# Kernel optimization log

Measured on AMD Instinct MI355X. Metric: run time of the kernel, lower is better.

Reference implementation:

```python
import jax, jax.numpy as jnp
import numpy as np

B, S, E, H = 2, 2048, 1024, 16
D = E // H  # head_dim = 64


def _rope_angles(seq_len, d, dtype=jnp.float32):
    # standard RoPE frequencies: theta_i = 10000^{-2i/d}
    inv_freq = 1.0 / (10000.0 ** (jnp.arange(0, d, 2, dtype=dtype) / d))  # [d/2]
    pos = jnp.arange(seq_len, dtype=dtype)                                # [S]
    ang = pos[:, None] * inv_freq[None, :]                                # [S, d/2]
    ang = jnp.concatenate([ang, ang], axis=-1)                            # [S, d]
    return jnp.cos(ang), jnp.sin(ang)


def _rotate_half(t):
    t1, t2 = jnp.split(t, 2, axis=-1)
    return jnp.concatenate([-t2, t1], axis=-1)


def _apply_rope(t, cos, sin):
    # t: [B, H, S, D]; cos/sin: [S, D]
    return t * cos[None, None, :, :] + _rotate_half(t) * sin[None, None, :, :]


def setup_inputs() -> dict:
    key = jax.random.key(0)
    ks = jax.random.split(key, 6)
    x = jax.random.normal(ks[0], (B, S, E), dtype=jnp.float32)
    mask = jnp.tril(jnp.ones((S, S), dtype=bool))  # causal: True = attend
    scale = 1.0 / np.sqrt(E)
    Wq = jax.random.normal(ks[1], (E, E), dtype=jnp.float32) * scale
    Wk = jax.random.normal(ks[2], (E, E), dtype=jnp.float32) * scale
    Wv = jax.random.normal(ks[3], (E, E), dtype=jnp.float32) * scale
    Wo = jax.random.normal(ks[4], (E, E), dtype=jnp.float32) * scale
    z = jnp.zeros((E,), dtype=jnp.float32)
    return {"x": x, "mask": mask, "Wq": Wq, "bq": z, "Wk": Wk, "bk": z,
            "Wv": Wv, "bv": z, "Wo": Wo, "bo": z}


def reference(x, mask, Wq, bq, Wk, bk, Wv, bv, Wo, bo):
    b, s, e = x.shape
    # QKV projections (nn.Linear convention: y = x @ W.T + b)
    def proj(W, bias):
        y = jnp.einsum('bse,fe->bsf', x, W) + bias
        return y.reshape(b, s, H, D).transpose(0, 2, 1, 3)  # [B,H,S,D]
    q, k, v = proj(Wq, bq), proj(Wk, bk), proj(Wv, bv)
    # RoPE on q and k (per-head rotary over head_dim)
    cos, sin = _rope_angles(s, D, dtype=x.dtype)
    q = _apply_rope(q, cos, sin)
    k = _apply_rope(k, cos, sin)
    # SDPA with boolean mask (True = attend)
    scores = jnp.einsum('bhqd,bhkd->bhqk', q, k) / jnp.sqrt(jnp.asarray(D, x.dtype))
    neg = jnp.asarray(jnp.finfo(x.dtype).min, x.dtype)
    scores = jnp.where(mask[None, None, :, :], scores, neg)
    attn = jax.nn.softmax(scores, axis=-1)
    out = jnp.einsum('bhqk,bhkd->bhqd', attn, v)          # [B,H,S,D]
    out = out.transpose(0, 2, 1, 3).reshape(b, s, e)       # [B,S,E]
    return jnp.einsum('bse,fe->bsf', out, Wo) + bo
```

## Files before the change

### kernel.cpp

```cpp
#include <hip/hip_runtime.h>
#include <hip/hip_bf16.h>

typedef unsigned short u16;
typedef unsigned int u32;
typedef __bf16 bf16x8 __attribute__((ext_vector_type(8)));
typedef float f32x4 __attribute__((ext_vector_type(4)));

#define S_LEN 2048
#define NHEAD 16
#define HDIM  64
#define EMB   1024
#define BATCH 2

__device__ __forceinline__ float bf2f(u16 u) {
  union { unsigned int i; float f; } c; c.i = ((unsigned int)u) << 16; return c.f;
}
__device__ __forceinline__ u16 f2bf(float f) {
  union { float f; unsigned int i; } c; c.f = f;
  unsigned int i = c.i;
  return (u16)((i + 0x7FFFu + ((i >> 16) & 1u)) >> 16);
}
__device__ __forceinline__ u16 f2bf_trunc(float f) {
  union { float f; unsigned int i; } c; c.f = f;
  return (u16)(c.i >> 16);
}
__device__ __forceinline__ f32x4 mfma16(bf16x8 a, bf16x8 b, f32x4 c) {
  return __builtin_amdgcn_mfma_f32_16x16x32_bf16(a, b, c, 0, 0, 0);
}
__device__ __forceinline__ void cp16(const u16* g, u16* l) {
  __builtin_amdgcn_global_load_lds(
      (const __attribute__((address_space(1))) u32*)g,
      (__attribute__((address_space(3))) u32*)l, 16, 0, 0);
}

__global__ __launch_bounds__(256) void convert_kernel(
    const void* __restrict__ x, const void* __restrict__ Wq,
    const void* __restrict__ Wk, const void* __restrict__ Wv,
    const void* __restrict__ Wo,
    u16* __restrict__ xb, u16* __restrict__ wqb, u16* __restrict__ wkb,
    u16* __restrict__ wvb, u16* __restrict__ wob,
    int* __restrict__ flag, float2* __restrict__ tab)
{
  __shared__ int s_flag;
  if (threadIdx.x == 0) s_flag = 0;
  __syncthreads();
  {
    const u16* xs = (const u16*)x;
    u16 w0 = xs[threadIdx.x * 2], w1 = xs[threadIdx.x * 2 + 1];
    if ((((w0 >> 7) & 0xFF) >= 0xC0) || (((w1 >> 7) & 0xFF) >= 0xC0))
      atomicOr(&s_flag, 1);
  }
  __syncthreads();
  const int f32io = s_flag;
  if (blockIdx.x == 0 && threadIdx.x == 0) flag[0] = f32io;

  size_t gid = (size_t)blockIdx.x * 256 + threadIdx.x;
  size_t e = gid * 8;
  const void* src; u16* dst; size_t off;
  if (e < 4194304) { src = x; dst = xb; off = e; }
  else {
    size_t rr = e - 4194304;
    int j = (int)(rr >> 20); off = rr & 1048575;
    src = (j == 0) ? Wq : (j == 1) ? Wk : (j == 2) ? Wv : Wo;
    dst = (j == 0) ? wqb : (j == 1) ? wkb : (j == 2) ? wvb : wob;
  }
  if (f32io) {
    const float* s = (const float*)src + off;
    float4 a = *(const float4*)s;
    float4 b2 = *(const float4*)(s + 4);
    ushort4 u0; u0.x = f2bf(a.x); u0.y = f2bf(a.y); u0.z = f2bf(a.z); u0.w = f2bf(a.w);
    ushort4 u1; u1.x = f2bf(b2.x); u1.y = f2bf(b2.y); u1.z = f2bf(b2.z); u1.w = f2bf(b2.w);
    *(ushort4*)(dst + off) = u0;
    *(ushort4*)(dst + off + 4) = u1;
  } else {
    *(uint4*)(dst + off) = *(const uint4*)((const u16*)src + off);
  }

  if (blockIdx.x < 256) {
    int id = blockIdx.x * 256 + threadIdx.x;
    int s = id >> 5, i = id & 31;
    float f = exp2f(-(float)i * 0.41524101186092029f);
    float ang = (float)s * f;
    tab[id] = make_float2(cosf(ang), sinf(ang));
  }
}

__device__ __forceinline__ void gemm_core_db(
    const u16* __restrict__ A, const u16* __restrict__ W,
    int m0, int n0, int t, f32x4 (&acc)[4][4],
    u16* __restrict__ Ash, u16* __restrict__ Bsh)
{
  const int lane = t & 63, lr = lane & 15, quad = lane >> 4;
  const int wv = t >> 6;
  const int wm = (wv & 1) * 64, wn = (wv >> 1) * 64;
  const int r0 = t >> 2, c0 = (t & 3) * 8;
  const int r1 = (t + 256) >> 2, c1 = (t & 3) * 8;
  const int lds0 = (t & 192) * 8;
  const int lds1 = (256 + (t & 192)) * 8;
  const u16* gA0 = A + (size_t)(m0 + r0) * 1024 + c0;
  const u16* gA1 = A + (size_t)(m0 + r1) * 1024 + c1;
  const u16* gB0 = W + (size_t)(n0 + r0) * 1024 + c0;
  const u16* gB1 = W + (size_t)(n0 + r1) * 1024 + c1;

  cp16(gA0, Ash + lds0); cp16(gA1, Ash + lds1);
  cp16(gB0, Bsh + lds0); cp16(gB1, Bsh + lds1);
  __syncthreads();

  for (int kt = 0; kt < 1024; kt += 32) {
    const int cur = (kt >> 5) & 1;
    const u16* Ac = Ash + cur * 4096;
    const u16* Bc = Bsh + cur * 4096;
    bf16x8 af[4], bfr[4];
#pragma unroll
    for (int mi = 0; mi < 4; ++mi)
      af[mi] = *(const bf16x8*)(Ac + (wm + mi * 16 + lr) * 32 + quad * 8);
#pragma unroll
    for (int ni = 0; ni < 4; ++ni)
      bfr[ni] = *(const bf16x8*)(Bc + (wn + ni * 16 + lr) * 32 + quad * 8);
    if (kt + 32 < 1024) {
      u16* An = Ash + (1 - cur) * 4096;
      u16* Bn = Bsh + (1 - cur) * 4096;
      cp16(gA0 + kt + 32, An + lds0); cp16(gA1 + kt + 32, An + lds1);
      cp16(gB0 + kt + 32, Bn + lds0); cp16(gB1 + kt + 32, Bn + lds1);
    }
#pragma unroll
    for (int mi = 0; mi < 4; ++mi)
#pragma unroll
      for (int ni = 0; ni < 4; ++ni)
        acc[mi][ni] = mfma16(af[mi], bfr[ni], acc[mi][ni]);
    __syncthreads();
  }
}

__device__ __forceinline__ void gemm_epilogue(
    int mode, int f32io, f32x4 (&acc)[4][4],
    const void* biasvp, void* outvp, int m0, int n0, int t,
    const float2* __restrict__ tab)
{
  const int lane = t & 63, lr = lane & 15, quad = lane >> 4;
  const int wv = t >> 6;
  const int wm = (wv & 1) * 64, wn = (wv >> 1) * 64;
  const float* biasf = (const float*)biasvp;
  const u16* biasb = (const u16*)biasvp;
#define BIASV(n) (f32io ? biasf[(n)] : bf2f(biasb[(n)]))
  if (mode == 1) {
    u16* Out = (u16*)outvp;
#pragma unroll
    for (int mi = 0; mi < 4; ++mi) {
#pragma unroll
      for (int r = 0; r < 4; ++r) {
        int mm = m0 + wm + mi * 16 + quad * 4 + r;
        int s = mm & (S_LEN - 1), b = mm >> 11;
        float2 cs0 = tab[s * 32 + lr];
        float2 cs1 = tab[s * 32 + 16 + lr];
#pragma unroll
        for (int ni = 0; ni < 4; ++ni) {
          int n = n0 + wn + ni * 16 + lr;
          int h = n >> 6, d = n & 63;
          float v  = acc[mi][ni][r]     + BIASV(n);
          float vp = acc[mi][ni ^ 2][r] + BIASV(n ^ 32);
          float rot = (d < 32) ? -vp : vp;
          float cc = (ni & 1) ? cs1.x : cs0.x;
          float ss = (ni & 1) ? cs1.y : cs0.y;
          size_t off = (((size_t)(b * NHEAD + h)) * S_LEN + s) * HDIM + d;
          Out[off] = f2bf(v * cc + rot * ss);
        }
      }
    }
  } else if (mode == 2) {
    u16* Out = (u16*)outvp;
#pragma unroll
    for (int mi = 0; mi < 4; ++mi) {
      int mm = m0 + wm + mi * 16 + quad * 4;
      int s = mm & (S_LEN - 1), b = mm >> 11;
#pragma unroll
      for (int ni = 0; ni < 4; ++ni) {
        int n = n0 + wn + ni * 16 + lr;
        int h = n >> 6, d = n & 63;
        float bv = BIASV(n);
        u16 p0 = f2bf(acc[mi][ni][0] + bv);
        u16 p1 = f2bf(acc[mi][ni][1] + bv);
        u16 p2 = f2bf(acc[mi][ni][2] + bv);
        u16 p3 = f2bf(acc[mi][ni][3] + bv);
        uint2 pk = make_uint2((u32)p0 | ((u32)p1 << 16),
                              (u32)p2 | ((u32)p3 << 16));
        size_t off = (((size_t)(b * NHEAD + h)) * HDIM + d) * S_LEN + s;
        *(uint2*)(Out + off) = pk;
      }
    }
  }
#undef BIASV
}

__global__ __launch_bounds__(256) void gemm_qkv(
    const u16* __restrict__ A, const u16* __restrict__ Wq,
    const u16* __restrict__ Wk, const u16* __restrict__ Wv,
    const void* bq, const void* bk, const void* bv,
    u16* qo, u16* ko, u16* vo, const int* __restrict__ dflag,
    const float2* __restrict__ tab)
{
  alignas(16) __shared__ u16 Ash[2 * 128 * 32];
  alignas(16) __shared__ u16 Bsh[2 * 128 * 32];
  const int wsel = blockIdx.x >> 3;
  const u16* W = (wsel == 0) ? Wq : (wsel == 1) ? Wk : Wv;
  const void* bias = (wsel == 0) ? bq : (wsel == 1) ? bk : bv;
  void* out = (wsel == 0) ? (void*)qo : (wsel == 1) ? (void*)ko : (void*)vo;
  const int mode = (wsel == 2) ? 2 : 1;
  const int m0 = blockIdx.y * 128, n0 = (blockIdx.x & 7) * 128;
  f32x4 acc[4][4];
  const f32x4 zero4 = {0.f, 0.f, 0.f, 0.f};
#pragma unroll
  for (int i = 0; i < 4; ++i)
#pragma unroll
    for (int j = 0; j < 4; ++j) acc[i][j] = zero4;
  gemm_core_db(A, W, m0, n0, threadIdx.x, acc, Ash, Bsh);
  gemm_epilogue(mode, dflag[0], acc, bias, out, m0, n0, threadIdx.x, tab);
}

__global__ __launch_bounds__(256) void gemm_out(
    const u16* __restrict__ A, const u16* __restrict__ W,
    const void* bias, void* out, const int* __restrict__ dflag)
{
  alignas(16) __shared__ u16 Ash[2 * 64 * 32];
  alignas(16) __shared__ u16 Bsh[2 * 128 * 32];
  const int t = threadIdx.x, lane = t & 63, wv = t >> 6;
  const int lr = lane & 15, quad = lane >> 4;
  const int m0 = blockIdx.y * 64, n0 = blockIdx.x * 128;
  const int wm = (wv & 1) * 32, wn = (wv >> 1) * 64;
  const int f32io = dflag[0];

  const int r0 = t >> 2, c0 = (t & 3) * 8;
  const int r1 = (t + 256) >> 2;
  const int lds0 = (t & 192) * 8;
  const int lds1 = (256 + (t & 192)) * 8;
  const u16* gA0 = A + (size_t)(m0 + (r0 & 63)) * 1024 + c0;
  const u16* gB0 = W + (size_t)(n0 + r0) * 1024 + c0;
  const u16* gB1 = W + (size_t)(n0 + r1) * 1024 + c0;

  f32x4 acc[2][4];
  const f32x4 zero4 = {0.f, 0.f, 0.f, 0.f};
#pragma unroll
  for (int i = 0; i < 2; ++i)
#pragma unroll
    for (int j = 0; j < 4; ++j) acc[i][j] = zero4;

  cp16(gA0, Ash + lds0);
  cp16(gB0, Bsh + lds0); cp16(gB1, Bsh + lds1);
  __syncthreads();

  for (int kt = 0; kt < 1024; kt += 32) {
    const int cur = (kt >> 5) & 1;
    const u16* Ac = Ash + cur * 2048;
    const u16* Bc = Bsh + cur * 4096;
    bf16x8 af[2], bfr[4];
#pragma unroll
    for (int mi = 0; mi < 2; ++mi)
      af[mi] = *(const bf16x8*)(Ac + (wm + mi * 16 + lr) * 32 + quad * 8);
#pragma unroll
    for (int ni = 0; ni < 4; ++ni)
      bfr[ni] = *(const bf16x8*)(Bc + (wn + ni * 16 + lr) * 32 + quad * 8);
    if (kt + 32 < 1024) {
      u16* An = Ash + (1 - cur) * 2048;
      u16* Bn = Bsh + (1 - cur) * 4096;
      cp16(gA0 + kt + 32, An + lds0);
      cp16(gB0 + kt + 32, Bn + lds0); cp16(gB1 + kt + 32, Bn + lds1);
    }
#pragma unroll
    for (int mi = 0; mi < 2; ++mi)
#pragma unroll
      for (int ni = 0; ni < 4; ++ni)
        acc[mi][ni] = mfma16(af[mi], bfr[ni], acc[mi][ni]);
    __syncthreads();
  }

  const float* biasf = (const float*)bias;
  const u16* biasb = (const u16*)bias;
  float* Outf = (float*)out;
  u16* Outb = (u16*)out;
#pragma unroll
  for (int mi = 0; mi < 2; ++mi) {
#pragma unroll
    for (int r = 0; r < 4; ++r) {
      int mm = m0 + wm + mi * 16 + quad * 4 + r;
#pragma unroll
      for (int ni = 0; ni < 4; ++ni) {
        int n = n0 + wn + ni * 16 + lr;
        float bv = f32io ? biasf[n] : bf2f(biasb[n]);
        float v = acc[mi][ni][r] + bv;
        size_t off = (size_t)mm * 1024 + n;
        if (f32io) Outf[off] = v; else Outb[off] = f2bf(v);
      }
    }
  }
}

__device__ __forceinline__ void attn_phase(
    const bf16x8 (&qf)[2], f32x4 (&oacc)[4], float& lsum,
    u16 (&Ksh)[64][72], u16 (&Vsh)[64][72], u16 (&Psh)[4][16][72],
    int kv0, int q0w, bool diag, int lr, int quad, int wv)
{
  const f32x4 zero4 = {0.f, 0.f, 0.f, 0.f};
  f32x4 sc[4];
#pragma unroll
  for (int ni = 0; ni < 4; ++ni) {
    bf16x8 kf0 = *(const bf16x8*)&Ksh[ni * 16 + lr][quad * 8];
    bf16x8 kf1 = *(const bf16x8*)&Ksh[ni * 16 + lr][32 + quad * 8];
    f32x4 z = zero4;
    z = mfma16(kf0, qf[0], z);
    z = mfma16(kf1, qf[1], z);
    sc[ni] = z;
  }
  const int qa = q0w + lr;
  if (diag) {
#pragma unroll
    for (int ni = 0; ni < 4; ++ni)
#pragma unroll
      for (int r = 0; r < 4; ++r) {
        float sarg = sc[ni][r] * 0.18033688f - 21.64042561f;
        if (kv0 + ni * 16 + quad * 4 + r > qa) sarg = -1e4f;
        float p = exp2f(sarg);
        sc[ni][r] = p;
        lsum += p;
      }
  } else {
#pragma unroll
    for (int ni = 0; ni < 4; ++ni)
#pragma unroll
      for (int r = 0; r < 4; ++r) {
        float p = exp2f(sc[ni][r] * 0.18033688f - 21.64042561f);
        sc[ni][r] = p;
        lsum += p;
      }
  }
#pragma unroll
  for (int ni = 0; ni < 4; ++ni) {
    u32 lo = (u32)f2bf_trunc(sc[ni][0]) | ((u32)f2bf_trunc(sc[ni][1]) << 16);
    u32 hi = (u32)f2bf_trunc(sc[ni][2]) | ((u32)f2bf_trunc(sc[ni][3]) << 16);
    *(uint2*)&Psh[wv][lr][ni * 16 + quad * 4] = make_uint2(lo, hi);
  }
  bf16x8 pa0 = *(const bf16x8*)&Psh[wv][lr][quad * 8];
  bf16x8 pa1 = *(const bf16x8*)&Psh[wv][lr][32 + quad * 8];
#pragma unroll
  for (int oni = 0; oni < 4; ++oni) {
    bf16x8 vf0 = *(const bf16x8*)&Vsh[oni * 16 + lr][quad * 8];
    bf16x8 vf1 = *(const bf16x8*)&Vsh[oni * 16 + lr][32 + quad * 8];
    oacc[oni] = mfma16(pa0, vf0, oacc[oni]);
    oacc[oni] = mfma16(pa1, vf1, oacc[oni]);
  }
}

__device__ __forceinline__ void attn_finish(
    f32x4 (&oacc)[4], float lsum, u16* __restrict__ O,
    int bh, int q0w, int lr, int quad)
{
  const int b = bh >> 4, h = bh & 15;
  lsum += __shfl_xor(lsum, 16);
  lsum += __shfl_xor(lsum, 32);
  const float inv = 1.f / lsum;
#pragma unroll
  for (int r = 0; r < 4; ++r) {
    const float scale = __shfl(inv, quad * 4 + r);
#pragma unroll
    for (int oni = 0; oni < 4; ++oni) {
      int s = q0w + quad * 4 + r;
      int e = h * HDIM + oni * 16 + lr;
      O[((size_t)(b * S_LEN + s)) * EMB + e] = f2bf(oacc[oni][r] * scale);
    }
  }
}

__global__ __launch_bounds__(256) void attn_kernel(
    const u16* __restrict__ Q, const u16* __restrict__ Kr,
    const u16* __restrict__ Vt, u16* __restrict__ O)
{
  alignas(16) __shared__ u16 Ksh[64][72];
  alignas(16) __shared__ u16 Vsh[64][72];
  alignas(16) __shared__ u16 Psh[4][16][72];
  const int t = threadIdx.x, lane = t & 63, wv = t >> 6;
  const int lr = lane & 15, quad = lane >> 4;
  const int bh = blockIdx.y;
  const int xs = blockIdx.x;
  const int myTile = (xs >> 4) ? (xs & 15) : 31 - (xs & 15);
  const int q0w = myTile * 64 + wv * 16;
  const size_t base = (size_t)bh * S_LEN * HDIM;

  bf16x8 qf[2];
  {
    const u16* qrow = Q + base + (size_t)(q0w + lr) * HDIM + quad * 8;
    qf[0] = *(const bf16x8*)qrow;
    qf[1] = *(const bf16x8*)(qrow + 32);
  }

  f32x4 oacc[4];
  float lsum = 0.f;
  const f32x4 zero4 = {0.f, 0.f, 0.f, 0.f};
#pragma unroll
  for (int i = 0; i < 4; ++i) oacc[i] = zero4;

  const int rr = t >> 3, cc = (t & 7) * 8;
  uint4 krg0 = *(const uint4*)(Kr + base + (size_t)rr * HDIM + cc);
  uint4 krg1 = *(const uint4*)(Kr + base + (size_t)(rr + 32) * HDIM + cc);
  uint4 vrg0 = *(const uint4*)(Vt + base + (size_t)rr * S_LEN + cc);
  uint4 vrg1 = *(const uint4*)(Vt + base + (size_t)(rr + 32) * S_LEN + cc);

  for (int j = 0; j <= myTile; ++j) {
    __syncthreads();
    *(uint4*)&Ksh[rr][cc] = krg0;
    *(uint4*)&Ksh[rr + 32][cc] = krg1;
    *(uint4*)&Vsh[rr][cc] = vrg0;
    *(uint4*)&Vsh[rr + 32][cc] = vrg1;
    __syncthreads();
    if (j < myTile) {
      const int kv1 = (j + 1) * 64;
      krg0 = *(const uint4*)(Kr + base + (size_t)(kv1 + rr) * HDIM + cc);
      krg1 = *(const uint4*)(Kr + base + (size_t)(kv1 + rr + 32) * HDIM + cc);
      vrg0 = *(const uint4*)(Vt + base + (size_t)rr * S_LEN + kv1 + cc);
      vrg1 = *(const uint4*)(Vt + base + (size_t)(rr + 32) * S_LEN + kv1 + cc);
    }
    attn_phase(qf, oacc, lsum, Ksh, Vsh, Psh, j * 64, q0w, j == myTile,
               lr, quad, wv);
  }

  attn_finish(oacc, lsum, O, bh, q0w, lr, quad);
}

extern "C" void kernel_launch(void* const* d_in, const int* in_sizes, int n_in,
                              void* d_out, int out_size, void* d_ws, size_t ws_size,
                              hipStream_t stream) {
  const void* x  = d_in[0];
  const void* Wq = d_in[2]; const void* bq = d_in[3];
  const void* Wk = d_in[4]; const void* bk = d_in[5];
  const void* Wv = d_in[6]; const void* bv = d_in[7];
  const void* Wo = d_in[8]; const void* bo = d_in[9];

  char* ws = (char*)d_ws;
  int* flag = (int*)ws;
  u16* xb  = (u16*)(ws + 256);
  u16* qws = xb  + 4194304;
  u16* kws = qws + 4194304;
  u16* vws = kws + 4194304;
  u16* wqb = vws + 4194304;
  u16* wkb = wqb + 1048576;
  u16* wvb = wkb + 1048576;
  u16* wob = wvb + 1048576;
  float2* tab = (float2*)(wob + 1048576);
  u16* ows = xb;

  convert_kernel<<<4096, 256, 0, stream>>>(x, Wq, Wk, Wv, Wo,
                                           xb, wqb, wkb, wvb, wob, flag, tab);
  gemm_qkv<<<dim3(24, 32), 256, 0, stream>>>(xb, wqb, wkb, wvb,
                                             bq, bk, bv, qws, kws, vws, flag, tab);
  attn_kernel<<<dim3(32, 32), 256, 0, stream>>>(qws, kws, vws, ows);
  gemm_out<<<dim3(8, 64), 256, 0, stream>>>(ows, wob, bo, d_out, flag);
}
```

Baseline: 241.4 us.

## Pair causal query tiles per 512-thread block with split-KV work balancing

Each attention block now handles two query tiles (qtA and 31-qtA) with 8 waves. Once group A's short tile finishes, its waves split the remaining long-tile KV blocks with group B by halves of the key dimension, and the partial outputs are merged through shared memory. K/V shared tiles are double-buffered so there is one barrier per iteration instead of two. This targets causal load imbalance and the cost of synchronisation, at the price of higher register and LDS use per block and an extra reduction step at the end.

Result: faster. 208.5 us (-13.6%).

```diff
diff --git a/kernel.cpp b/kernel.cpp
--- a/kernel.cpp
+++ b/kernel.cpp
@@ -296,8 +296,9 @@
 
 __device__ __forceinline__ void attn_phase(
     const bf16x8 (&qf)[2], f32x4 (&oacc)[4], float& lsum,
-    u16 (&Ksh)[64][72], u16 (&Vsh)[64][72], u16 (&Psh)[4][16][72],
-    int kv0, int q0w, bool diag, int lr, int quad, int wv)
+    const u16 (*__restrict__ Ksh)[72], const u16 (*__restrict__ Vsh)[72],
+    u16 (*__restrict__ Pw)[72],
+    int kv0, int q0w, bool diag, int lr, int quad)
 {
   const f32x4 zero4 = {0.f, 0.f, 0.f, 0.f};
   f32x4 sc[4];
@@ -336,10 +337,10 @@
   for (int ni = 0; ni < 4; ++ni) {
     u32 lo = (u32)f2bf_trunc(sc[ni][0]) | ((u32)f2bf_trunc(sc[ni][1]) << 16);
     u32 hi = (u32)f2bf_trunc(sc[ni][2]) | ((u32)f2bf_trunc(sc[ni][3]) << 16);
-    *(uint2*)&Psh[wv][lr][ni * 16 + quad * 4] = make_uint2(lo, hi);
-  }
-  bf16x8 pa0 = *(const bf16x8*)&Psh[wv][lr][quad * 8];
-  bf16x8 pa1 = *(const bf16x8*)&Psh[wv][lr][32 + quad * 8];
+    *(uint2*)&Pw[lr][ni * 16 + quad * 4] = make_uint2(lo, hi);
+  }
+  bf16x8 pa0 = *(const bf16x8*)&Pw[lr][quad * 8];
+  bf16x8 pa1 = *(const bf16x8*)&Pw[lr][32 + quad * 8];
 #pragma unroll
   for (int oni = 0; oni < 4; ++oni) {
     bf16x8 vf0 = *(const bf16x8*)&Vsh[oni * 16 + lr][quad * 8];
@@ -349,6 +350,60 @@
   }
 }
 
+__device__ __forceinline__ void attn_phase_half(
+    const bf16x8 (&qf)[2], f32x4 (&oacc)[4], float& lsum,
+    const u16 (*__restrict__ Ksh)[72], const u16 (*__restrict__ Vsh)[72],
+    u16 (*__restrict__ Pw)[72],
+    int kv0, int q0w, bool diag, int half, int lr, int quad)
+{
+  const f32x4 zero4 = {0.f, 0.f, 0.f, 0.f};
+  f32x4 sc[2];
+#pragma unroll
+  for (int i = 0; i < 2; ++i) {
+    const int ni = half * 2 + i;
+    bf16x8 kf0 = *(const bf16x8*)&Ksh[ni * 16 + lr][quad * 8];
+    bf16x8 kf1 = *(const bf16x8*)&Ksh[ni * 16 + lr][32 + quad * 8];
+    f32x4 z = zero4;
+    z = mfma16(kf0, qf[0], z);
+    z = mfma16(kf1, qf[1], z);
+    sc[i] = z;
+  }
+  const int qa = q0w + lr;
+  if (diag) {
+#pragma unroll
+    for (int i = 0; i < 2; ++i)
+#pragma unroll
+      for (int r = 0; r < 4; ++r) {
+        float sarg = sc[i][r] * 0.18033688f - 21.64042561f;
+        if (kv0 + (half * 2 + i) * 16 + quad * 4 + r > qa) sarg = -1e4f;
+        float p = exp2f(sarg);
+        sc[i][r] = p;
+        lsum += p;
+      }
+  } else {
+#pragma unroll
+    for (int i = 0; i < 2; ++i)
+#pragma unroll
+      for (int r = 0; r < 4; ++r) {
+        float p = exp2f(sc[i][r] * 0.18033688f - 21.64042561f);
+        sc[i][r] = p;
+        lsum += p;
+      }
+  }
+#pragma unroll
+  for (int i = 0; i < 2; ++i) {
+    u32 lo = (u32)f2bf_trunc(sc[i][0]) | ((u32)f2bf_trunc(sc[i][1]) << 16);
+    u32 hi = (u32)f2bf_trunc(sc[i][2]) | ((u32)f2bf_trunc(sc[i][3]) << 16);
+    *(uint2*)&Pw[lr][(half * 2 + i) * 16 + quad * 4] = make_uint2(lo, hi);
+  }
+  bf16x8 pa = *(const bf16x8*)&Pw[lr][half * 32 + quad * 8];
+#pragma unroll
+  for (int oni = 0; oni < 4; ++oni) {
+    bf16x8 vf = *(const bf16x8*)&Vsh[oni * 16 + lr][half * 32 + quad * 8];
+    oacc[oni] = mfma16(pa, vf, oacc[oni]);
+  }
+}
+
 __device__ __forceinline__ void attn_finish(
     f32x4 (&oacc)[4], float lsum, u16* __restrict__ O,
     int bh, int q0w, int lr, int quad)
@@ -369,59 +424,87 @@
   }
 }
 
-__global__ __launch_bounds__(256) void attn_kernel(
+__global__ __launch_bounds__(512, 4) void attn_kernel(
     const u16* __restrict__ Q, const u16* __restrict__ Kr,
     const u16* __restrict__ Vt, u16* __restrict__ O)
 {
-  alignas(16) __shared__ u16 Ksh[64][72];
-  alignas(16) __shared__ u16 Vsh[64][72];
-  alignas(16) __shared__ u16 Psh[4][16][72];
+  alignas(16) __shared__ u16 Kdb[2][64][72];
+  alignas(16) __shared__ u16 Vdb[2][64][72];
+  alignas(16) __shared__ u16 Psh[8][16][72];
   const int t = threadIdx.x, lane = t & 63, wv = t >> 6;
   const int lr = lane & 15, quad = lane >> 4;
   const int bh = blockIdx.y;
-  const int xs = blockIdx.x;
-  const int myTile = (xs >> 4) ? (xs & 15) : 31 - (xs & 15);
-  const int q0w = myTile * 64 + wv * 16;
+  const int qtA = blockIdx.x;
+  const int qtB = 31 - qtA;
+  const bool grpA = (wv < 4);
+  const int q0own = (grpA ? qtA : qtB) * 64 + (wv & 3) * 16;
+  const int q0B = qtB * 64 + (wv & 3) * 16;
   const size_t base = (size_t)bh * S_LEN * HDIM;
 
-  bf16x8 qf[2];
+  bf16x8 qfO[2], qfH[2];
   {
-    const u16* qrow = Q + base + (size_t)(q0w + lr) * HDIM + quad * 8;
-    qf[0] = *(const bf16x8*)qrow;
-    qf[1] = *(const bf16x8*)(qrow + 32);
-  }
-
-  f32x4 oacc[4];
-  float lsum = 0.f;
+    const u16* qrow = Q + base + (size_t)(q0own + lr) * HDIM + quad * 8;
+    qfO[0] = *(const bf16x8*)qrow;
+    qfO[1] = *(const bf16x8*)(qrow + 32);
+  }
+  if (grpA) {
+    const u16* qrow = Q + base + (size_t)(q0B + lr) * HDIM + quad * 8;
+    qfH[0] = *(const bf16x8*)qrow;
+    qfH[1] = *(const bf16x8*)(qrow + 32);
+  } else { qfH[0] = qfO[0]; qfH[1] = qfO[1]; }
+
+  f32x4 oacc0[4], oacc1[4];
+  float lsum0 = 0.f, lsum1 = 0.f;
   const f32x4 zero4 = {0.f, 0.f, 0.f, 0.f};
 #pragma unroll
-  for (int i = 0; i < 4; ++i) oacc[i] = zero4;
+  for (int i = 0; i < 4; ++i) { oacc0[i] = zero4; oacc1[i] = zero4; }
 
   const int rr = t >> 3, cc = (t & 7) * 8;
-  uint4 krg0 = *(const uint4*)(Kr + base + (size_t)rr * HDIM + cc);
-  uint4 krg1 = *(const uint4*)(Kr + base + (size_t)(rr + 32) * HDIM + cc);
-  uint4 vrg0 = *(const uint4*)(Vt + base + (size_t)rr * S_LEN + cc);
-  uint4 vrg1 = *(const uint4*)(Vt + base + (size_t)(rr + 32) * S_LEN + cc);
-
-  for (int j = 0; j <= myTile; ++j) {
+  uint4 krg = *(const uint4*)(Kr + base + (size_t)rr * HDIM + cc);
+  uint4 vrg = *(const uint4*)(Vt + base + (size_t)rr * S_LEN + cc);
+
+  for (int j = 0; j <= qtB; ++j) {
+    const int cur = j & 1;
+    *(uint4*)&Kdb[cur][rr][cc] = krg;
+    *(uint4*)&Vdb[cur][rr][cc] = vrg;
     __syncthreads();
-    *(uint4*)&Ksh[rr][cc] = krg0;
-    *(uint4*)&Ksh[rr + 32][cc] = krg1;
-    *(uint4*)&Vsh[rr][cc] = vrg0;
-    *(uint4*)&Vsh[rr + 32][cc] = vrg1;
-    __syncthreads();
-    if (j < myTile) {
+    if (j < qtB) {
       const int kv1 = (j + 1) * 64;
-      krg0 = *(const uint4*)(Kr + base + (size_t)(kv1 + rr) * HDIM + cc);
-      krg1 = *(const uint4*)(Kr + base + (size_t)(kv1 + rr + 32) * HDIM + cc);
-      vrg0 = *(const uint4*)(Vt + base + (size_t)rr * S_LEN + kv1 + cc);
-      vrg1 = *(const uint4*)(Vt + base + (size_t)(rr + 32) * S_LEN + kv1 + cc);
-    }
-    attn_phase(qf, oacc, lsum, Ksh, Vsh, Psh, j * 64, q0w, j == myTile,
-               lr, quad, wv);
-  }
-
-  attn_finish(oacc, lsum, O, bh, q0w, lr, quad);
+      krg = *(const uint4*)(Kr + base + (size_t)(kv1 + rr) * HDIM + cc);
+      vrg = *(const uint4*)(Vt + base + (size_t)rr * S_LEN + kv1 + cc);
+    }
+    if (j <= qtA) {
+      attn_phase(qfO, oacc0, lsum0, Kdb[cur], Vdb[cur], Psh[wv],
+                 j * 64, q0own, grpA && (j == qtA), lr, quad);
+    } else if (grpA) {
+      attn_phase_half(qfH, oacc1, lsum1, Kdb[cur], Vdb[cur], Psh[wv],
+                      j * 64, q0B, j == qtB, 1, lr, quad);
+    } else {
+      attn_phase_half(qfO, oacc0, lsum0, Kdb[cur], Vdb[cur], Psh[wv],
+                      j * 64, q0B, j == qtB, 0, lr, quad);
+    }
+  }
+
+  __syncthreads();
+  if (grpA) {
+    float* dst = (float*)&Psh[0][0][0] + (size_t)(wv * 64 + lane) * 17;
+#pragma unroll
+    for (int oni = 0; oni < 4; ++oni)
+#pragma unroll
+      for (int r = 0; r < 4; ++r) dst[oni * 4 + r] = oacc1[oni][r];
+    dst[16] = lsum1;
+  }
+  __syncthreads();
+  if (!grpA) {
+    const float* src =
+        (const float*)&Psh[0][0][0] + (size_t)((wv - 4) * 64 + lane) * 17;
+#pragma unroll
+    for (int oni = 0; oni < 4; ++oni)
+#pragma unroll
+      for (int r = 0; r < 4; ++r) oacc0[oni][r] += src[oni * 4 + r];
+    lsum0 += src[16];
+  }
+  attn_finish(oacc0, lsum0, O, bh, q0own, lr, quad);
 }
 
 extern "C" void kernel_launch(void* const* d_in, const int* in_sizes, int n_in,
@@ -450,6 +533,6 @@
                                            xb, wqb, wkb, wvb, wob, flag, tab);
   gemm_qkv<<<dim3(24, 32), 256, 0, stream>>>(xb, wqb, wkb, wvb,
                                              bq, bk, bv, qws, kws, vws, flag, tab);
-  attn_kernel<<<dim3(32, 32), 256, 0, stream>>>(qws, kws, vws, ows);
+  attn_kernel<<<dim3(16, 32), 512, 0, stream>>>(qws, kws, vws, ows);
   gemm_out<<<dim3(8, 64), 256, 0, stream>>>(ows, wob, bo, d_out, flag);
 }
```
